# Kernel optimization log

Hardware: AMD Instinct MI355X
Metric: run time of the kernel (lower is better)

Reference implementation:

```python
import jax, jax.numpy as jnp
import numpy as np

N, M, F, W = 600000, 300000, 128, 256  # points, masked points, grid feat_dim, net width


def _lin_init(k, fi, fo):
    k1, k2 = jax.random.split(k)
    s = 1.0 / np.sqrt(fi)
    return (jax.random.uniform(k1, (fi, fo), jnp.float32, -s, s),
            jax.random.uniform(k2, (fo,), jnp.float32, -s, s))


def setup_inputs() -> dict:
    key = jax.random.key(0)
    ks = jax.random.split(key, 24)
    # unique sorted indices emulate the boolean target_mask (static count M)
    idx = jnp.asarray(np.sort(np.random.RandomState(0).permutation(N)[:M]).astype(np.int32))
    inp = {
        "rays_pts_emb": jax.random.normal(ks[0], (N, 3), jnp.float32),
        "rotations_emb": jax.random.normal(ks[1], (N, 4), jnp.float32),
        "shs_emb": jax.random.normal(ks[2], (N, 16, 3), jnp.float32),
        "time_emb": jax.random.uniform(ks[3], (N, 1), jnp.float32),
        "h_emb": jax.random.uniform(ks[4], (N, 1), jnp.float32),
        "grid_sp": jax.random.normal(ks[5], (M, F), jnp.float32),
        "grid_st": jax.random.normal(ks[6], (M, F), jnp.float32),
        "idx": idx,
    }
    layers = [("sp", F, W), ("st", F, W), ("p1", W, W), ("p2", W, 9),
              ("r1", W, W), ("r2", W, 4), ("s1", W, W), ("s2", W, 48),
              ("w1", W, W), ("w2", W, 1), ("m1", W, W), ("m2", W, 1)]
    for i, (nm, fi, fo) in enumerate(layers):
        Wt, b = _lin_init(ks[7 + i], fi, fo)
        inp["W_" + nm] = Wt
        inp["b_" + nm] = b
    return inp


def _head(x, W1, b1, W2, b2):
    # nn.Sequential(ReLU, Linear, ReLU, Linear)
    h = jax.nn.relu(x)
    h = jax.nn.relu(h @ W1 + b1)
    return h @ W2 + b2


def reference(rays_pts_emb, rotations_emb, shs_emb, time_emb, h_emb, grid_sp, grid_st, idx,
              W_sp, b_sp, W_st, b_st, W_p1, b_p1, W_p2, b_p2, W_r1, b_r1, W_r2, b_r2,
              W_s1, b_s1, W_s2, b_s2, W_w1, b_w1, W_w2, b_w2, W_m1, b_m1, W_m2, b_m2):
    # encoders (Linear only, no activation)
    sp = grid_sp @ W_sp + b_sp            # [M, W]
    st = grid_st @ W_st + b_st            # [M, W]
    t = time_emb[0:1]                     # [1, 1]
    mint = 1.0 - t
    # position deformation: Bezier combination of 3 control offsets
    dx = _head(sp, W_p1, b_p1, W_p2, b_p2).reshape(-1, 3, 3)  # [M, 3, 3]
    delta = (3.0 * mint ** 2 * t * dx[:, 0]
             + 3.0 * mint * t ** 2 * dx[:, 1]
             + t ** 3 * dx[:, 2])                              # [M, 3]
    pts = rays_pts_emb.at[idx].add(delta)
    rotations = rotations_emb.at[idx].add(_head(st, W_r1, b_r1, W_r2, b_r2))
    shs = shs_emb.at[idx].add(_head(st, W_s1, b_s1, W_s2, b_s2).reshape(-1, 16, 3))
    # opacity gating
    w = _head(sp, W_w1, b_w1, W_w2, b_w2) ** 2                 # [M, 1]
    mu = jax.nn.sigmoid(_head(sp, W_m1, b_m1, W_m2, b_m2))     # [M, 1]
    opacity = h_emb.at[idx].set(h_emb[idx] * jnp.exp(-w * (t - mu) ** 2))
    return (pts, rotations, opacity, shs)
```

## Files before the change

### kernel.cpp

```cpp
#include <hip/hip_runtime.h>
#include <hip/hip_bf16.h>
#include <stdint.h>

#define M_ROWS 300000

typedef __attribute__((ext_vector_type(8)))  short bf16x8;
typedef __attribute__((ext_vector_type(16))) float f32x16;

union U4 { uint4 u; bf16x8 h; unsigned short us[8]; };

__device__ __forceinline__ unsigned short f2bf(float f) {
  union { float f; uint32_t u; } v; v.f = f;
  uint32_t r = v.u + 0x7fffu + ((v.u >> 16) & 1u);
  return (unsigned short)(r >> 16);
}
__device__ __forceinline__ uint32_t pk2(float lo, float hi) {
  return (uint32_t)f2bf(lo) | ((uint32_t)f2bf(hi) << 16);
}

#define T_SP 0
#define T_ST 64
#define T_P1 128
#define T_P2 256
#define T_R1 272
#define T_R2 400
#define T_S1 416
#define T_S2 544
#define T_W1 576
#define T_W2 704
#define T_M1 720
#define T_M2 848
#define T_TOT 864

__global__ void prep_w(const float* Wsp, const float* Wst, const float* Wp1, const float* Wp2,
                       const float* Wr1, const float* Wr2, const float* Ws1, const float* Ws2,
                       const float* Ww1, const float* Ww2, const float* Wm1, const float* Wm2,
                       uint4* ws) {
  int b = blockIdx.x, l = threadIdx.x;
  const int starts[12] = {T_SP,T_ST,T_P1,T_P2,T_R1,T_R2,T_S1,T_S2,T_W1,T_W2,T_M1,T_M2};
  const int Ks[12]     = {128,128,256,256,256,256,256,256,256,256,256,256};
  const int Cos[12]    = {256,256,256,9,256,4,256,48,256,1,256,1};
  const float* Wp[12]  = {Wsp,Wst,Wp1,Wp2,Wr1,Wr2,Ws1,Ws2,Ww1,Ww2,Wm1,Wm2};
  int m = 0;
  #pragma unroll
  for (int i = 1; i < 12; ++i) if (b >= starts[i]) m = i;
  int local = b - starts[m];
  int KT = Ks[m] >> 4;
  int n0 = local / KT, k0 = local - n0 * KT;
  int col = n0 * 32 + (l & 31);
  int kbase = k0 * 16 + (l >> 5) * 8;
  const float* W = Wp[m];
  int Co = Cos[m];
  U4 pk;
  #pragma unroll
  for (int j = 0; j < 8; ++j) {
    float v = (col < Co) ? W[(size_t)(kbase + j) * Co + col] : 0.0f;
    pk.us[j] = f2bf(v);
  }
  ws[(size_t)b * 64 + l] = pk.u;
}

__global__ void copy_emb(const float4* pts, const float4* rot, const float4* h,
                         const float4* shs, float4* out) {
  long long stride = (long long)gridDim.x * blockDim.x;
  for (long long i = (long long)blockIdx.x * blockDim.x + threadIdx.x; i < 8400000LL; i += stride) {
    float4 v;
    if (i < 450000)        v = pts[i];
    else if (i < 1050000)  v = rot[i - 450000];
    else if (i < 1200000)  v = h[i - 1050000];
    else                   v = shs[i - 1200000];
    out[i] = v;
  }
}

#define LSTR 512
__device__ __forceinline__ int lds_addr(int row, int cb) {
  return row * LSTR + (cb ^ ((row & 15) << 4));
}

__device__ __forceinline__ void loadX(const float* grid, int row0, int t, char* buf) {
  #pragma unroll
  for (int i = 0; i < 4; ++i) {
    int fi = i * 512 + t;
    int row = fi >> 5;
    int c4 = fi & 31;
    int gr = row0 + row; gr = gr < M_ROWS ? gr : (M_ROWS - 1);
    float4 v = ((const float4*)grid)[(size_t)gr * 32 + c4];
    ushort4 p;
    p.x = f2bf(v.x); p.y = f2bf(v.y); p.z = f2bf(v.z); p.w = f2bf(v.w);
    *(ushort4*)(buf + lds_addr(row, c4 * 8)) = p;
  }
}

__device__ __forceinline__ void pre8(U4 (&d)[8], const uint4* base, int lane) {
  #pragma unroll
  for (int i = 0; i < 8; ++i) d[i].u = base[(size_t)i * 64 + lane];
}
__device__ __forceinline__ void pre4(U4 (&d)[8], const uint4* base, int lane) {
  #pragma unroll
  for (int i = 0; i < 4; ++i) d[i].u = base[(size_t)i * 64 + lane];
}
__device__ __forceinline__ void pre_s2(U4 (&d)[8], const uint4* wt, int kq, int lane) {
  #pragma unroll
  for (int kk = 0; kk < 4; ++kk)
    #pragma unroll
    for (int n = 0; n < 2; ++n)
      d[kk * 2 + n].u = wt[(size_t)((n * 16 + kq * 4 + kk) * 64) + lane];
}

__device__ __forceinline__ void mm_big8T(U4 (&b)[8], const char* inb, int k0, int arow, int khalf,
                                         f32x16& acc0, f32x16& acc1) {
  #pragma unroll
  for (int k = 0; k < 8; ++k) {
    bf16x8 x0 = *(const bf16x8*)(inb + lds_addr(arow, (k0 + k) * 32 + khalf));
    bf16x8 x1 = *(const bf16x8*)(inb + lds_addr(32 + arow, (k0 + k) * 32 + khalf));
    acc0 = __builtin_amdgcn_mfma_f32_32x32x16_bf16(b[k].h, x0, acc0, 0, 0, 0);
    acc1 = __builtin_amdgcn_mfma_f32_32x32x16_bf16(b[k].h, x1, acc1, 0, 0, 0);
  }
}

__device__ __forceinline__ void store_actT(char* outb, const float* bias, int wave, int lane,
                                           const f32x16& acc0, const f32x16& acc1) {
  const int xr = lane & 31;
  const int cb0 = wave * 32 + 4 * (lane >> 5);
  #pragma unroll
  for (int run = 0; run < 4; ++run) {
    const int c0 = cb0 + 8 * run;
    const float4 bv = *(const float4*)(bias + c0);
    uint2 w0, w1;
    w0.x = pk2(fmaxf(acc0[run * 4 + 0] + bv.x, 0.0f), fmaxf(acc0[run * 4 + 1] + bv.y, 0.0f));
    w0.y = pk2(fmaxf(acc0[run * 4 + 2] + bv.z, 0.0f), fmaxf(acc0[run * 4 + 3] + bv.w, 0.0f));
    w1.x = pk2(fmaxf(acc1[run * 4 + 0] + bv.x, 0.0f), fmaxf(acc1[run * 4 + 1] + bv.y, 0.0f));
    w1.y = pk2(fmaxf(acc1[run * 4 + 2] + bv.z, 0.0f), fmaxf(acc1[run * 4 + 3] + bv.w, 0.0f));
    *(uint2*)(outb + lds_addr(xr, c0 * 2)) = w0;
    *(uint2*)(outb + lds_addr(32 + xr, c0 * 2)) = w1;
  }
}

__device__ __forceinline__ void mm_head1(U4 (&b)[8], const char* inb, int rg, int kq, int khalf,
                                         int lane, f32x16& acc) {
  const int arow = rg * 32 + (lane & 31);
  #pragma unroll
  for (int kk = 0; kk < 4; ++kk) {
    bf16x8 a = *(const bf16x8*)(inb + lds_addr(arow, (kq * 4 + kk) * 32 + khalf));
    acc = __builtin_amdgcn_mfma_f32_32x32x16_bf16(a, b[kk].h, acc, 0, 0, 0);
  }
}

template<int COLS>
__device__ __forceinline__ void head_atomic(float* outsm, int rg, int lane, const f32x16& acc) {
  int col = lane & 31;
  if (col < COLS) {
    #pragma unroll
    for (int q = 0; q < 16; ++q) {
      int row = rg * 32 + (q & 3) + 8 * (q >> 2) + 4 * (lane >> 5);
      atomicAdd(&outsm[row * COLS + col], acc[q]);
    }
  }
}

__device__ __forceinline__ void rot_atomic_global(const f32x16& acc, int rg, int kq, int lane,
                                                  const int* sidx, int row0, const float* b_r2,
                                                  float* out) {
  int col = lane & 31;
  if (col < 4) {
    float bb = (kq == 0) ? b_r2[col] : 0.0f;
    #pragma unroll
    for (int q = 0; q < 16; ++q) {
      int row = rg * 32 + (q & 3) + 8 * (q >> 2) + 4 * (lane >> 5);
      if (row0 + row < M_ROWS) {
        atomicAdd(out + 1800000 + (size_t)sidx[row] * 4 + col, acc[q] + bb);
      }
    }
  }
}

__device__ __forceinline__ void shs_atomic_global(const f32x16& a0, const f32x16& a1,
                                                  int rg, int kq, int lane,
                                                  const int* sidx, int row0, const float* b_s2,
                                                  float* out) {
  int c = lane & 31;
  float bb0 = (kq == 0) ? b_s2[c] : 0.0f;
  float bb1 = (kq == 0 && c < 16) ? b_s2[32 + c] : 0.0f;
  #pragma unroll
  for (int q = 0; q < 16; ++q) {
    int row = rg * 32 + (q & 3) + 8 * (q >> 2) + 4 * (lane >> 5);
    if (row0 + row < M_ROWS) {
      size_t base = 4800000 + (size_t)sidx[row] * 48;
      atomicAdd(out + base + c, a0[q] + bb0);
      if (c < 16) atomicAdd(out + base + 32 + c, a1[q] + bb1);
    }
  }
}

__global__ void __launch_bounds__(512, 4) deform_main(
    const float* grid_sp, const float* grid_st, const int* idx,
    const float* rays, const float* rotq, const float* shs_in,
    const float* time_emb, const float* h_emb,
    const uint4* ws,
    const float* b_sp, const float* b_st, const float* b_p1, const float* b_p2,
    const float* b_r1, const float* b_r2, const float* b_s1, const float* b_s2,
    const float* b_w1, const float* b_w2, const float* b_m1, const float* b_m2,
    float* out) {
  __shared__ char bufA[32768];
  __shared__ char bufB[32768];
  __shared__ float smf[704];
  __shared__ int sidx[64];
  float* dxb = smf;
  float* wb  = smf + 576;
  float* mub = smf + 640;

  const int t = threadIdx.x;
  const int lane = t & 63;
  const int wave = t >> 6;
  const int rg = wave & 1;
  const int kq = wave >> 1;
  const int arow = lane & 31;
  const int khalf = (lane >> 5) * 16;
  const int row0 = blockIdx.x * 64;
  const float tt = time_emb[0];

  U4 b0[8], b1[8];
  pre8(b0, ws + (size_t)(T_SP + wave * 8) * 64, lane);

  if (t < 64) { int gr = row0 + t; sidx[t] = idx[gr < M_ROWS ? gr : (M_ROWS - 1)]; }
  if (t < 512) smf[t] = 0.0f;
  if (t < 192) smf[512 + t] = 0.0f;
  loadX(grid_sp, row0, t, bufA);
  __syncthreads();

  {
    f32x16 a0 = (f32x16)0.0f, a1 = (f32x16)0.0f;
    pre8(b1, ws + (size_t)(T_P1 + wave * 16) * 64, lane);
    __builtin_amdgcn_s_setprio(1);
    mm_big8T(b0, bufA, 0, arow, khalf, a0, a1);
    __builtin_amdgcn_s_setprio(0);
    store_actT(bufB, b_sp, wave, lane, a0, a1);
  }
  __syncthreads();

  {
    f32x16 a0 = (f32x16)0.0f, a1 = (f32x16)0.0f;
    pre8(b0, ws + (size_t)(T_P1 + wave * 16 + 8) * 64, lane);
    __builtin_amdgcn_s_setprio(1);
    mm_big8T(b1, bufB, 0, arow, khalf, a0, a1);
    __builtin_amdgcn_s_setprio(0);
    pre4(b1, ws + (size_t)(T_P2 + kq * 4) * 64, lane);
    __builtin_amdgcn_s_setprio(1);
    mm_big8T(b0, bufB, 8, arow, khalf, a0, a1);
    __builtin_amdgcn_s_setprio(0);
    store_actT(bufA, b_p1, wave, lane, a0, a1);
  }
  __syncthreads();

  {
    f32x16 hacc = (f32x16)0.0f;
    pre8(b0, ws + (size_t)(T_W1 + wave * 16) * 64, lane);
    __builtin_amdgcn_s_setprio(1);
    mm_head1(b1, bufA, rg, kq, khalf, lane, hacc);
    __builtin_amdgcn_s_setprio(0);
    head_atomic<9>(dxb, rg, lane, hacc);
  }
  __syncthreads();

  {
    f32x16 a0 = (f32x16)0.0f, a1 = (f32x16)0.0f;
    pre8(b1, ws + (size_t)(T_W1 + wave * 16 + 8) * 64, lane);
    __builtin_amdgcn_s_setprio(1);
    mm_big8T(b0, bufB, 0, arow, khalf, a0, a1);
    __builtin_amdgcn_s_setprio(0);
    pre4(b0, ws + (size_t)(T_W2 + kq * 4) * 64, lane);
    __builtin_amdgcn_s_setprio(1);
    mm_big8T(b1, bufB, 8, arow, khalf, a0, a1);
    __builtin_amdgcn_s_setprio(0);
    store_actT(bufA, b_w1, wave, lane, a0, a1);
  }
  __syncthreads();

  {
    f32x16 hacc = (f32x16)0.0f;
    pre8(b1, ws + (size_t)(T_M1 + wave * 16) * 64, lane);
    __builtin_amdgcn_s_setprio(1);
    mm_head1(b0, bufA, rg, kq, khalf, lane, hacc);
    __builtin_amdgcn_s_setprio(0);
    head_atomic<1>(wb, rg, lane, hacc);
  }
  __syncthreads();

  {
    f32x16 a0 = (f32x16)0.0f, a1 = (f32x16)0.0f;
    pre8(b0, ws + (size_t)(T_M1 + wave * 16 + 8) * 64, lane);
    __builtin_amdgcn_s_setprio(1);
    mm_big8T(b1, bufB, 0, arow, khalf, a0, a1);
    __builtin_amdgcn_s_setprio(0);
    pre4(b1, ws + (size_t)(T_M2 + kq * 4) * 64, lane);
    __builtin_amdgcn_s_setprio(1);
    mm_big8T(b0, bufB, 8, arow, khalf, a0, a1);
    __builtin_amdgcn_s_setprio(0);
    store_actT(bufA, b_m1, wave, lane, a0, a1);
  }
  __syncthreads();

  float pr = 0.0f, hv = 0.0f;
  {
    if (t < 256) {
      int row = t >> 2, sub = t & 3;
      int g = sidx[row];
      if (sub < 3) pr = rays[(size_t)g * 3 + sub]; else hv = h_emb[g];
    }
    loadX(grid_st, row0, t, bufB);
    f32x16 hacc = (f32x16)0.0f;
    __builtin_amdgcn_s_setprio(1);
    mm_head1(b1, bufA, rg, kq, khalf, lane, hacc);
    __builtin_amdgcn_s_setprio(0);
    pre8(b0, ws + (size_t)(T_ST + wave * 8) * 64, lane);
    head_atomic<1>(mub, rg, lane, hacc);
  }
  __syncthreads();

  {
    f32x16 a0 = (f32x16)0.0f, a1 = (f32x16)0.0f;
    pre8(b1, ws + (size_t)(T_R1 + wave * 16) * 64, lane);
    __builtin_amdgcn_s_setprio(1);
    mm_big8T(b0, bufB, 0, arow, khalf, a0, a1);
    __builtin_amdgcn_s_setprio(0);
    store_actT(bufA, b_st, wave, lane, a0, a1);
    if (t < 256) {
      int row = t >> 2, sub = t & 3;
      int gr = row0 + row;
      if (gr < M_ROWS) {
        int g = sidx[row];
        if (sub < 3) {
          float mt = 1.0f - tt;
          float c0 = 3.0f * mt * mt * tt, c1 = 3.0f * mt * tt * tt, c2 = tt * tt * tt;
          float d0 = dxb[row * 9 + sub]     + b_p2[sub];
          float d1 = dxb[row * 9 + 3 + sub] + b_p2[3 + sub];
          float d2 = dxb[row * 9 + 6 + sub] + b_p2[6 + sub];
          out[(size_t)g * 3 + sub] = pr + (c0 * d0 + c1 * d1 + c2 * d2);
        } else {
          float wr = wb[row] + b_w2[0];
          float mr = mub[row] + b_m2[0];
          float mu = 1.0f / (1.0f + expf(-mr));
          float dtm = tt - mu;
          out[4200000 + (size_t)g] = hv * expf(-(wr * wr) * dtm * dtm);
        }
      }
    }
  }
  __syncthreads();

  {
    f32x16 a0 = (f32x16)0.0f, a1 = (f32x16)0.0f;
    pre8(b0, ws + (size_t)(T_R1 + wave * 16 + 8) * 64, lane);
    __builtin_amdgcn_s_setprio(1);
    mm_big8T(b1, bufA, 0, arow, khalf, a0, a1);
    __builtin_amdgcn_s_setprio(0);
    pre4(b1, ws + (size_t)(T_R2 + kq * 4) * 64, lane);
    __builtin_amdgcn_s_setprio(1);
    mm_big8T(b0, bufA, 8, arow, khalf, a0, a1);
    __builtin_amdgcn_s_setprio(0);
    store_actT(bufB, b_r1, wave, lane, a0, a1);
  }
  __syncthreads();

  {
    f32x16 hacc = (f32x16)0.0f;
    pre8(b0, ws + (size_t)(T_S1 + wave * 16) * 64, lane);
    __builtin_amdgcn_s_setprio(1);
    mm_head1(b1, bufB, rg, kq, khalf, lane, hacc);
    __builtin_amdgcn_s_setprio(0);
    rot_atomic_global(hacc, rg, kq, lane, sidx, row0, b_r2, out);
  }
  __syncthreads();

  {
    f32x16 a0 = (f32x16)0.0f, a1 = (f32x16)0.0f;
    pre8(b1, ws + (size_t)(T_S1 + wave * 16 + 8) * 64, lane);
    __builtin_amdgcn_s_setprio(1);
    mm_big8T(b0, bufA, 0, arow, khalf, a0, a1);
    __builtin_amdgcn_s_setprio(0);
    pre_s2(b0, ws + (size_t)T_S2 * 64, kq, lane);
    __builtin_amdgcn_s_setprio(1);
    mm_big8T(b1, bufA, 8, arow, khalf, a0, a1);
    __builtin_amdgcn_s_setprio(0);
    store_actT(bufB, b_s1, wave, lane, a0, a1);
  }
  __syncthreads();

  {
    f32x16 h0 = (f32x16)0.0f, h1 = (f32x16)0.0f;
    const int ar = rg * 32 + (lane & 31);
    __builtin_amdgcn_s_setprio(1);
    #pragma unroll
    for (int kk = 0; kk < 4; ++kk) {
      bf16x8 a = *(const bf16x8*)(bufB + lds_addr(ar, (kq * 4 + kk) * 32 + khalf));
      h0 = __builtin_amdgcn_mfma_f32_32x32x16_bf16(a, b0[kk * 2 + 0].h, h0, 0, 0, 0);
      h1 = __builtin_amdgcn_mfma_f32_32x32x16_bf16(a, b0[kk * 2 + 1].h, h1, 0, 0, 0);
    }
    __builtin_amdgcn_s_setprio(0);
    shs_atomic_global(h0, h1, rg, kq, lane, sidx, row0, b_s2, out);
  }
}

extern "C" void kernel_launch(void* const* d_in, const int* in_sizes, int n_in,
                              void* d_out, int out_size, void* d_ws, size_t ws_size,
                              hipStream_t stream) {
  const float* rays     = (const float*)d_in[0];
  const float* rotq     = (const float*)d_in[1];
  const float* shs      = (const float*)d_in[2];
  const float* time_emb = (const float*)d_in[3];
  const float* h_emb    = (const float*)d_in[4];
  const float* grid_sp  = (const float*)d_in[5];
  const float* grid_st  = (const float*)d_in[6];
  const int*   idx      = (const int*)d_in[7];
  uint4* ws = (uint4*)d_ws;

  prep_w<<<T_TOT, 64, 0, stream>>>(
      (const float*)d_in[8],  (const float*)d_in[10], (const float*)d_in[12], (const float*)d_in[14],
      (const float*)d_in[16], (const float*)d_in[18], (const float*)d_in[20], (const float*)d_in[22],
      (const float*)d_in[24], (const float*)d_in[26], (const float*)d_in[28], (const float*)d_in[30],
      ws);

  copy_emb<<<2048, 256, 0, stream>>>((const float4*)rays, (const float4*)rotq,
                                     (const float4*)h_emb, (const float4*)shs, (float4*)d_out);

  deform_main<<<(M_ROWS + 63) / 64, 512, 0, stream>>>(
      grid_sp, grid_st, idx, rays, rotq, shs, time_emb, h_emb, ws,
      (const float*)d_in[9],  (const float*)d_in[11], (const float*)d_in[13], (const float*)d_in[15],
      (const float*)d_in[17], (const float*)d_in[19], (const float*)d_in[21], (const float*)d_in[23],
      (const float*)d_in[25], (const float*)d_in[27], (const float*)d_in[29], (const float*)d_in[31],
      (float*)d_out);
}
```

Before: 741.0 us.

## Split big-GEMM rows across 16 waves with 1024-thread blocks

```diff
diff --git a/kernel.cpp b/kernel.cpp
--- a/kernel.cpp
+++ b/kernel.cpp
@@ -80,8 +80,8 @@
 
 __device__ __forceinline__ void loadX(const float* grid, int row0, int t, char* buf) {
   #pragma unroll
-  for (int i = 0; i < 4; ++i) {
-    int fi = i * 512 + t;
+  for (int i = 0; i < 2; ++i) {
+    int fi = i * 1024 + t;
     int row = fi >> 5;
     int c4 = fi & 31;
     int gr = row0 + row; gr = gr < M_ROWS ? gr : (M_ROWS - 1);
@@ -108,32 +108,28 @@
       d[kk * 2 + n].u = wt[(size_t)((n * 16 + kq * 4 + kk) * 64) + lane];
 }
 
-__device__ __forceinline__ void mm_big8T(U4 (&b)[8], const char* inb, int k0, int arow, int khalf,
-                                         f32x16& acc0, f32x16& acc1) {
+__device__ __forceinline__ void mm_big8H(U4 (&b)[8], const char* inb, int k0, int arowg, int khalf,
+                                         f32x16& acc) {
   #pragma unroll
   for (int k = 0; k < 8; ++k) {
-    bf16x8 x0 = *(const bf16x8*)(inb + lds_addr(arow, (k0 + k) * 32 + khalf));
-    bf16x8 x1 = *(const bf16x8*)(inb + lds_addr(32 + arow, (k0 + k) * 32 + khalf));
-    acc0 = __builtin_amdgcn_mfma_f32_32x32x16_bf16(b[k].h, x0, acc0, 0, 0, 0);
-    acc1 = __builtin_amdgcn_mfma_f32_32x32x16_bf16(b[k].h, x1, acc1, 0, 0, 0);
-  }
-}
-
-__device__ __forceinline__ void store_actT(char* outb, const float* bias, int wave, int lane,
-                                           const f32x16& acc0, const f32x16& acc1) {
-  const int xr = lane & 31;
-  const int cb0 = wave * 32 + 4 * (lane >> 5);
+    bf16x8 x = *(const bf16x8*)(inb + lds_addr(arowg, (k0 + k) * 32 + khalf));
+    acc = __builtin_amdgcn_mfma_f32_32x32x16_bf16(b[k].h, x, acc, 0, 0, 0);
+  }
+}
+
+__device__ __forceinline__ void store_actTH(char* outb, const float* bias, int ct, int rh, int lane,
+                                            const f32x16& acc) {
+  const int xr = rh * 32 + (lane & 31);
+  const int cb0 = ct * 32 + 4 * (lane >> 5);
   #pragma unroll
   for (int run = 0; run < 4; ++run) {
-    const int c0 = cb0 + 8 * run;
+    const int rr = (run + (lane >> 3)) & 3;
+    const int c0 = cb0 + 8 * rr;
     const float4 bv = *(const float4*)(bias + c0);
-    uint2 w0, w1;
-    w0.x = pk2(fmaxf(acc0[run * 4 + 0] + bv.x, 0.0f), fmaxf(acc0[run * 4 + 1] + bv.y, 0.0f));
-    w0.y = pk2(fmaxf(acc0[run * 4 + 2] + bv.z, 0.0f), fmaxf(acc0[run * 4 + 3] + bv.w, 0.0f));
-    w1.x = pk2(fmaxf(acc1[run * 4 + 0] + bv.x, 0.0f), fmaxf(acc1[run * 4 + 1] + bv.y, 0.0f));
-    w1.y = pk2(fmaxf(acc1[run * 4 + 2] + bv.z, 0.0f), fmaxf(acc1[run * 4 + 3] + bv.w, 0.0f));
-    *(uint2*)(outb + lds_addr(xr, c0 * 2)) = w0;
-    *(uint2*)(outb + lds_addr(32 + xr, c0 * 2)) = w1;
+    uint2 w;
+    w.x = pk2(fmaxf(acc[rr * 4 + 0] + bv.x, 0.0f), fmaxf(acc[rr * 4 + 1] + bv.y, 0.0f));
+    w.y = pk2(fmaxf(acc[rr * 4 + 2] + bv.z, 0.0f), fmaxf(acc[rr * 4 + 3] + bv.w, 0.0f));
+    *(uint2*)(outb + lds_addr(xr, c0 * 2)) = w;
   }
 }
 
@@ -193,7 +189,7 @@
   }
 }
 
-__global__ void __launch_bounds__(512, 4) deform_main(
+__global__ void __launch_bounds__(1024, 8) deform_main(
     const float* grid_sp, const float* grid_st, const int* idx,
     const float* rays, const float* rotq, const float* shs_in,
     const float* time_emb, const float* h_emb,
@@ -213,91 +209,96 @@
   const int t = threadIdx.x;
   const int lane = t & 63;
   const int wave = t >> 6;
+  const int ct = wave & 7;
+  const int rh = wave >> 3;
   const int rg = wave & 1;
   const int kq = wave >> 1;
-  const int arow = lane & 31;
+  const int arowg = rh * 32 + (lane & 31);
   const int khalf = (lane >> 5) * 16;
   const int row0 = blockIdx.x * 64;
   const float tt = time_emb[0];
 
   U4 b0[8], b1[8];
-  pre8(b0, ws + (size_t)(T_SP + wave * 8) * 64, lane);
+  pre8(b0, ws + (size_t)(T_SP + ct * 8) * 64, lane);
 
   if (t < 64) { int gr = row0 + t; sidx[t] = idx[gr < M_ROWS ? gr : (M_ROWS - 1)]; }
-  if (t < 512) smf[t] = 0.0f;
-  if (t < 192) smf[512 + t] = 0.0f;
+  if (t < 704) smf[t] = 0.0f;
   loadX(grid_sp, row0, t, bufA);
   __syncthreads();
 
   {
-    f32x16 a0 = (f32x16)0.0f, a1 = (f32x16)0.0f;
-    pre8(b1, ws + (size_t)(T_P1 + wave * 16) * 64, lane);
-    __builtin_amdgcn_s_setprio(1);
-    mm_big8T(b0, bufA, 0, arow, khalf, a0, a1);
-    __builtin_amdgcn_s_setprio(0);
-    store_actT(bufB, b_sp, wave, lane, a0, a1);
-  }
-  __syncthreads();
-
-  {
-    f32x16 a0 = (f32x16)0.0f, a1 = (f32x16)0.0f;
-    pre8(b0, ws + (size_t)(T_P1 + wave * 16 + 8) * 64, lane);
-    __builtin_amdgcn_s_setprio(1);
-    mm_big8T(b1, bufB, 0, arow, khalf, a0, a1);
-    __builtin_amdgcn_s_setprio(0);
-    pre4(b1, ws + (size_t)(T_P2 + kq * 4) * 64, lane);
-    __builtin_amdgcn_s_setprio(1);
-    mm_big8T(b0, bufB, 8, arow, khalf, a0, a1);
-    __builtin_amdgcn_s_setprio(0);
-    store_actT(bufA, b_p1, wave, lane, a0, a1);
-  }
-  __syncthreads();
-
-  {
-    f32x16 hacc = (f32x16)0.0f;
-    pre8(b0, ws + (size_t)(T_W1 + wave * 16) * 64, lane);
-    __builtin_amdgcn_s_setprio(1);
-    mm_head1(b1, bufA, rg, kq, khalf, lane, hacc);
-    __builtin_amdgcn_s_setprio(0);
-    head_atomic<9>(dxb, rg, lane, hacc);
-  }
-  __syncthreads();
-
-  {
-    f32x16 a0 = (f32x16)0.0f, a1 = (f32x16)0.0f;
-    pre8(b1, ws + (size_t)(T_W1 + wave * 16 + 8) * 64, lane);
-    __builtin_amdgcn_s_setprio(1);
-    mm_big8T(b0, bufB, 0, arow, khalf, a0, a1);
-    __builtin_amdgcn_s_setprio(0);
-    pre4(b0, ws + (size_t)(T_W2 + kq * 4) * 64, lane);
-    __builtin_amdgcn_s_setprio(1);
-    mm_big8T(b1, bufB, 8, arow, khalf, a0, a1);
-    __builtin_amdgcn_s_setprio(0);
-    store_actT(bufA, b_w1, wave, lane, a0, a1);
-  }
-  __syncthreads();
-
-  {
-    f32x16 hacc = (f32x16)0.0f;
-    pre8(b1, ws + (size_t)(T_M1 + wave * 16) * 64, lane);
-    __builtin_amdgcn_s_setprio(1);
-    mm_head1(b0, bufA, rg, kq, khalf, lane, hacc);
-    __builtin_amdgcn_s_setprio(0);
-    head_atomic<1>(wb, rg, lane, hacc);
-  }
-  __syncthreads();
-
-  {
-    f32x16 a0 = (f32x16)0.0f, a1 = (f32x16)0.0f;
-    pre8(b0, ws + (size_t)(T_M1 + wave * 16 + 8) * 64, lane);
-    __builtin_amdgcn_s_setprio(1);
-    mm_big8T(b1, bufB, 0, arow, khalf, a0, a1);
-    __builtin_amdgcn_s_setprio(0);
-    pre4(b1, ws + (size_t)(T_M2 + kq * 4) * 64, lane);
-    __builtin_amdgcn_s_setprio(1);
-    mm_big8T(b0, bufB, 8, arow, khalf, a0, a1);
-    __builtin_amdgcn_s_setprio(0);
-    store_actT(bufA, b_m1, wave, lane, a0, a1);
+    f32x16 acc = (f32x16)0.0f;
+    pre8(b1, ws + (size_t)(T_P1 + ct * 16) * 64, lane);
+    __builtin_amdgcn_s_setprio(1);
+    mm_big8H(b0, bufA, 0, arowg, khalf, acc);
+    __builtin_amdgcn_s_setprio(0);
+    store_actTH(bufB, b_sp, ct, rh, lane, acc);
+  }
+  __syncthreads();
+
+  {
+    f32x16 acc = (f32x16)0.0f;
+    pre8(b0, ws + (size_t)(T_P1 + ct * 16 + 8) * 64, lane);
+    __builtin_amdgcn_s_setprio(1);
+    mm_big8H(b1, bufB, 0, arowg, khalf, acc);
+    __builtin_amdgcn_s_setprio(0);
+    if (wave < 8) pre4(b1, ws + (size_t)(T_P2 + kq * 4) * 64, lane);
+    __builtin_amdgcn_s_setprio(1);
+    mm_big8H(b0, bufB, 8, arowg, khalf, acc);
+    __builtin_amdgcn_s_setprio(0);
+    store_actTH(bufA, b_p1, ct, rh, lane, acc);
+  }
+  __syncthreads();
+
+  {
+    if (wave < 8) {
+      f32x16 hacc = (f32x16)0.0f;
+      __builtin_amdgcn_s_setprio(1);
+      mm_head1(b1, bufA, rg, kq, khalf, lane, hacc);
+      __builtin_amdgcn_s_setprio(0);
+      head_atomic<9>(dxb, rg, lane, hacc);
+    }
+    pre8(b0, ws + (size_t)(T_W1 + ct * 16) * 64, lane);
+  }
+  __syncthreads();
+
+  {
+    f32x16 acc = (f32x16)0.0f;
+    pre8(b1, ws + (size_t)(T_W1 + ct * 16 + 8) * 64, lane);
+    __builtin_amdgcn_s_setprio(1);
+    mm_big8H(b0, bufB, 0, arowg, khalf, acc);
+    __builtin_amdgcn_s_setprio(0);
+    if (wave < 8) pre4(b0, ws + (size_t)(T_W2 + kq * 4) * 64, lane);
+    __builtin_amdgcn_s_setprio(1);
+    mm_big8H(b1, bufB, 8, arowg, khalf, acc);
+    __builtin_amdgcn_s_setprio(0);
+    store_actTH(bufA, b_w1, ct, rh, lane, acc);
+  }
+  __syncthreads();
+
+  {
+    if (wave < 8) {
+      f32x16 hacc = (f32x16)0.0f;
+      __builtin_amdgcn_s_setprio(1);
+      mm_head1(b0, bufA, rg, kq, khalf, lane, hacc);
+      __builtin_amdgcn_s_setprio(0);
+      head_atomic<1>(wb, rg, lane, hacc);
+    }
+    pre8(b1, ws + (size_t)(T_M1 + ct * 16) * 64, lane);
+  }
+  __syncthreads();
+
+  {
+    f32x16 acc = (f32x16)0.0f;
+    pre8(b0, ws + (size_t)(T_M1 + ct * 16 + 8) * 64, lane);
+    __builtin_amdgcn_s_setprio(1);
+    mm_big8H(b1, bufB, 0, arowg, khalf, acc);
+    __builtin_amdgcn_s_setprio(0);
+    if (wave < 8) pre4(b1, ws + (size_t)(T_M2 + kq * 4) * 64, lane);
+    __builtin_amdgcn_s_setprio(1);
+    mm_big8H(b0, bufB, 8, arowg, khalf, acc);
+    __builtin_amdgcn_s_setprio(0);
+    store_actTH(bufA, b_m1, ct, rh, lane, acc);
   }
   __syncthreads();
 
@@ -309,22 +310,24 @@
       if (sub < 3) pr = rays[(size_t)g * 3 + sub]; else hv = h_emb[g];
     }
     loadX(grid_st, row0, t, bufB);
-    f32x16 hacc = (f32x16)0.0f;
-    __builtin_amdgcn_s_setprio(1);
-    mm_head1(b1, bufA, rg, kq, khalf, lane, hacc);
-    __builtin_amdgcn_s_setprio(0);
-    pre8(b0, ws + (size_t)(T_ST + wave * 8) * 64, lane);
-    head_atomic<1>(mub, rg, lane, hacc);
-  }
-  __syncthreads();
-
-  {
-    f32x16 a0 = (f32x16)0.0f, a1 = (f32x16)0.0f;
-    pre8(b1, ws + (size_t)(T_R1 + wave * 16) * 64, lane);
-    __builtin_amdgcn_s_setprio(1);
-    mm_big8T(b0, bufB, 0, arow, khalf, a0, a1);
-    __builtin_amdgcn_s_setprio(0);
-    store_actT(bufA, b_st, wave, lane, a0, a1);
+    if (wave < 8) {
+      f32x16 hacc = (f32x16)0.0f;
+      __builtin_amdgcn_s_setprio(1);
+      mm_head1(b1, bufA, rg, kq, khalf, lane, hacc);
+      __builtin_amdgcn_s_setprio(0);
+      head_atomic<1>(mub, rg, lane, hacc);
+    }
+    pre8(b0, ws + (size_t)(T_ST + ct * 8) * 64, lane);
+  }
+  __syncthreads();
+
+  {
+    f32x16 acc = (f32x16)0.0f;
+    pre8(b1, ws + (size_t)(T_R1 + ct * 16) * 64, lane);
+    __builtin_amdgcn_s_setprio(1);
+    mm_big8H(b0, bufB, 0, arowg, khalf, acc);
+    __builtin_amdgcn_s_setprio(0);
+    store_actTH(bufA, b_st, ct, rh, lane, acc);
     if (t < 256) {
       int row = t >> 2, sub = t & 3;
       int gr = row0 + row;
@@ -350,44 +353,46 @@
   __syncthreads();
 
   {
-    f32x16 a0 = (f32x16)0.0f, a1 = (f32x16)0.0f;
-    pre8(b0, ws + (size_t)(T_R1 + wave * 16 + 8) * 64, lane);
-    __builtin_amdgcn_s_setprio(1);
-    mm_big8T(b1, bufA, 0, arow, khalf, a0, a1);
-    __builtin_amdgcn_s_setprio(0);
-    pre4(b1, ws + (size_t)(T_R2 + kq * 4) * 64, lane);
-    __builtin_amdgcn_s_setprio(1);
-    mm_big8T(b0, bufA, 8, arow, khalf, a0, a1);
-    __builtin_amdgcn_s_setprio(0);
-    store_actT(bufB, b_r1, wave, lane, a0, a1);
-  }
-  __syncthreads();
-
-  {
-    f32x16 hacc = (f32x16)0.0f;
-    pre8(b0, ws + (size_t)(T_S1 + wave * 16) * 64, lane);
-    __builtin_amdgcn_s_setprio(1);
-    mm_head1(b1, bufB, rg, kq, khalf, lane, hacc);
-    __builtin_amdgcn_s_setprio(0);
-    rot_atomic_global(hacc, rg, kq, lane, sidx, row0, b_r2, out);
-  }
-  __syncthreads();
-
-  {
-    f32x16 a0 = (f32x16)0.0f, a1 = (f32x16)0.0f;
-    pre8(b1, ws + (size_t)(T_S1 + wave * 16 + 8) * 64, lane);
-    __builtin_amdgcn_s_setprio(1);
-    mm_big8T(b0, bufA, 0, arow, khalf, a0, a1);
-    __builtin_amdgcn_s_setprio(0);
-    pre_s2(b0, ws + (size_t)T_S2 * 64, kq, lane);
-    __builtin_amdgcn_s_setprio(1);
-    mm_big8T(b1, bufA, 8, arow, khalf, a0, a1);
-    __builtin_amdgcn_s_setprio(0);
-    store_actT(bufB, b_s1, wave, lane, a0, a1);
-  }
-  __syncthreads();
-
-  {
+    f32x16 acc = (f32x16)0.0f;
+    pre8(b0, ws + (size_t)(T_R1 + ct * 16 + 8) * 64, lane);
+    __builtin_amdgcn_s_setprio(1);
+    mm_big8H(b1, bufA, 0, arowg, khalf, acc);
+    __builtin_amdgcn_s_setprio(0);
+    if (wave < 8) pre4(b1, ws + (size_t)(T_R2 + kq * 4) * 64, lane);
+    __builtin_amdgcn_s_setprio(1);
+    mm_big8H(b0, bufA, 8, arowg, khalf, acc);
+    __builtin_amdgcn_s_setprio(0);
+    store_actTH(bufB, b_r1, ct, rh, lane, acc);
+  }
+  __syncthreads();
+
+  {
+    if (wave < 8) {
+      f32x16 hacc = (f32x16)0.0f;
+      __builtin_amdgcn_s_setprio(1);
+      mm_head1(b1, bufB, rg, kq, khalf, lane, hacc);
+      __builtin_amdgcn_s_setprio(0);
+      rot_atomic_global(hacc, rg, kq, lane, sidx, row0, b_r2, out);
+    }
+    pre8(b0, ws + (size_t)(T_S1 + ct * 16) * 64, lane);
+  }
+  __syncthreads();
+
+  {
+    f32x16 acc = (f32x16)0.0f;
+    pre8(b1, ws + (size_t)(T_S1 + ct * 16 + 8) * 64, lane);
+    __builtin_amdgcn_s_setprio(1);
+    mm_big8H(b0, bufA, 0, arowg, khalf, acc);
+    __builtin_amdgcn_s_setprio(0);
+    if (wave < 8) pre_s2(b0, ws + (size_t)T_S2 * 64, kq, lane);
+    __builtin_amdgcn_s_setprio(1);
+    mm_big8H(b1, bufA, 8, arowg, khalf, acc);
+    __builtin_amdgcn_s_setprio(0);
+    store_actTH(bufB, b_s1, ct, rh, lane, acc);
+  }
+  __syncthreads();
+
+  if (wave < 8) {
     f32x16 h0 = (f32x16)0.0f, h1 = (f32x16)0.0f;
     const int ar = rg * 32 + (lane & 31);
     __builtin_amdgcn_s_setprio(1);
@@ -424,7 +429,7 @@
   copy_emb<<<2048, 256, 0, stream>>>((const float4*)rays, (const float4*)rotq,
                                      (const float4*)h_emb, (const float4*)shs, (float4*)d_out);
 
-  deform_main<<<(M_ROWS + 63) / 64, 512, 0, stream>>>(
+  deform_main<<<(M_ROWS + 63) / 64, 1024, 0, stream>>>(
       grid_sp, grid_st, idx, rays, rotq, shs, time_emb, h_emb, ws,
       (const float*)d_in[9],  (const float*)d_in[11], (const float*)d_in[13], (const float*)d_in[15],
       (const float*)d_in[17], (const float*)d_in[19], (const float*)d_in[21], (const float*)d_in[23],
```

After: 2.778 ms. 275% more time.
